# Kernel optimization log

Measured on AMD Instinct MI355X. Metric: run time of the kernel, lower is better.

Reference implementation:

```python
import jax, jax.numpy as jnp
import numpy as np

N_EMBD = 384
BLOCK_SIZE = 256

def setup_inputs() -> dict:
    key = jax.random.key(0)
    k1, k2 = jax.random.split(key)
    B, T = 512, 256
    x = jax.random.normal(k1, (B, T, N_EMBD), dtype=jnp.float32)
    # nn.Linear(384, 192, bias=False): store as [in, out] so projection is x @ w
    w_qkv = jax.random.normal(k2, (N_EMBD, 3 * 64), dtype=jnp.float32) * (1.0 / np.sqrt(N_EMBD))
    return {"x": x, "w_qkv": w_qkv}

def reference(x, w_qkv):
    B, T, C = x.shape  # C == n_embd == 384
    qkv = jnp.einsum('btc,cd->btd', x, w_qkv)       # [B,T,3*hs]
    q, k, v = jnp.split(qkv, 3, axis=-1)            # each [B,T,hs]
    scale = 1.0 / jnp.sqrt(jnp.float32(C))          # NOTE: scales by full embed dim C, per source
    wei = jnp.einsum('btd,bsd->bts', q, k) * scale  # [B,T,T]
    causal = jnp.tril(jnp.ones((T, T), dtype=bool))
    wei = jnp.where(causal, wei, -jnp.inf)
    wei = jax.nn.softmax(wei, axis=-1)
    # dropout is identity in eval mode
    return jnp.einsum('bts,bsd->btd', wei, v)       # [B,T,hs]
```

## Files before the change

### kernel.cpp

```cpp
#include <hip/hip_runtime.h>


constexpr int B  = 512;
constexpr int T  = 256;
constexpr int C  = 384;
constexpr int HS = 64;
constexpr int NT = 192;
constexpr int VP = 264;
constexpr float SCALE = 0.05103103630798288f;
constexpr float QSC   = SCALE * 1.4426950408889634f;

typedef _Float16 f16x8 __attribute__((ext_vector_type(8)));
typedef _Float16 f16x4 __attribute__((ext_vector_type(4)));
typedef __fp16   fp16x2_raw __attribute__((ext_vector_type(2)));
typedef float    f32x4 __attribute__((ext_vector_type(4)));

#if defined(__has_builtin)
#if __has_builtin(__builtin_amdgcn_exp2f)
#define EXP2F(v) __builtin_amdgcn_exp2f(v)
#endif
#endif
#ifndef EXP2F
#define EXP2F(v) exp2f(v)
#endif

__global__ __launch_bounds__(256)
void wt_kernel(const float* __restrict__ w, _Float16* __restrict__ wt) {
    const int idx = blockIdx.x * 256 + threadIdx.x;
    if (idx < NT * C) {
        const int n = idx / C, k = idx % C;
        wt[idx] = (_Float16)w[k * NT + n];
    }
}

__global__ __launch_bounds__(512)
void fused_kernel(const float* __restrict__ x, const _Float16* __restrict__ wt,
                  float* __restrict__ out) {
    __shared__ __align__(16) char arena[NT * C * 2];
    _Float16* const QL  = (_Float16*)arena;
    _Float16* const KL  = (_Float16*)(arena + 32768);
    _Float16* const VTL = (_Float16*)(arena + 65536);

    const int tid  = threadIdx.x;
    const int lane = tid & 63, wv = tid >> 6;
    const int l15  = lane & 15, quad = lane >> 4;
    const int swz  = (l15 & 7) << 4;
    const int q16  = quad << 4;
    const float* xb = x + (long)blockIdx.x * T * C;

#pragma unroll
    for (int i = 0; i < 18; ++i) {
        const int u = tid + 512 * i;
        const int n = u / 48, sl = u - n * 48;
        const uint4 wv4 = *(const uint4*)((const char*)wt + (long)u * 16);
        *(uint4*)(arena + n * 768 + ((sl * 16) ^ ((n & 7) << 4))) = wv4;
    }

    const float* pA0 = xb + (wv * 32 + l15) * C + quad * 8;
    const float* pA1 = xb + (wv * 32 + 16 + l15) * C + quad * 8;

    f32x4 ax[2][2][2];
    ax[0][0][0] = *(const f32x4*)(pA0 + 0);
    ax[0][0][1] = *(const f32x4*)(pA0 + 4);
    ax[0][1][0] = *(const f32x4*)(pA1 + 0);
    ax[0][1][1] = *(const f32x4*)(pA1 + 4);

    f32x4 acc[2][12];
#pragma unroll
    for (int mi = 0; mi < 2; ++mi)
#pragma unroll
        for (int ni = 0; ni < 12; ++ni) acc[mi][ni] = (f32x4)0.f;

    int rowb[12];
#pragma unroll
    for (int ni = 0; ni < 12; ++ni) rowb[ni] = (ni * 16 + l15) * 768;

    __syncthreads();

#pragma unroll
    for (int t = 0; t < 12; ++t) {
        const int cur = t & 1, nxt = cur ^ 1;
        if (t < 11) {
            ax[nxt][0][0] = *(const f32x4*)(pA0 + (t + 1) * 32);
            ax[nxt][0][1] = *(const f32x4*)(pA0 + (t + 1) * 32 + 4);
            ax[nxt][1][0] = *(const f32x4*)(pA1 + (t + 1) * 32);
            ax[nxt][1][1] = *(const f32x4*)(pA1 + (t + 1) * 32 + 4);
        }
        f16x8 af[2];
#pragma unroll
        for (int mi = 0; mi < 2; ++mi) {
            union { fp16x2_raw h[4]; f16x8 v; } cu;
            cu.h[0] = __builtin_amdgcn_cvt_pkrtz(ax[cur][mi][0][0], ax[cur][mi][0][1]);
            cu.h[1] = __builtin_amdgcn_cvt_pkrtz(ax[cur][mi][0][2], ax[cur][mi][0][3]);
            cu.h[2] = __builtin_amdgcn_cvt_pkrtz(ax[cur][mi][1][0], ax[cur][mi][1][1]);
            cu.h[3] = __builtin_amdgcn_cvt_pkrtz(ax[cur][mi][1][2], ax[cur][mi][1][3]);
            af[mi] = cu.v;
        }
        const int col = ((t * 64) + q16) ^ swz;
#pragma unroll
        for (int ni = 0; ni < 12; ++ni) {
            const f16x8 bf = *(const f16x8*)(arena + rowb[ni] + col);
            acc[0][ni] = __builtin_amdgcn_mfma_f32_16x16x32_f16(af[0], bf, acc[0][ni], 0, 0, 0);
            acc[1][ni] = __builtin_amdgcn_mfma_f32_16x16x32_f16(af[1], bf, acc[1][ni], 0, 0, 0);
        }
    }

    __syncthreads();

#pragma unroll
    for (int mi = 0; mi < 2; ++mi) {
        const int t0 = wv * 32 + mi * 16 + quad * 4;
#pragma unroll
        for (int ni = 0; ni < 12; ++ni) {
            const int colbase = ni * 16;
            const int col = colbase + l15;
            if (colbase < 64) {
#pragma unroll
                for (int r = 0; r < 4; ++r) {
                    const int tq = t0 + r;
                    QL[(tq * HS + col) ^ ((tq & 7) << 3)] =
                        (_Float16)(acc[mi][ni][r] * QSC);
                }
            } else if (colbase < 128) {
#pragma unroll
                for (int r = 0; r < 4; ++r) {
                    const int tq = t0 + r;
                    KL[(tq * HS + (col - 64)) ^ ((tq & 7) << 3)] =
                        (_Float16)acc[mi][ni][r];
                }
            } else {
                f16x4 pv;
#pragma unroll
                for (int r = 0; r < 4; ++r) pv[r] = (_Float16)acc[mi][ni][r];
                *(f16x4*)&VTL[(col - 128) * VP + t0] = pv;
            }
        }
    }
    __syncthreads();

    float* ob = out + (long)blockIdx.x * T * HS;
#pragma unroll
    for (int pass = 0; pass < 2; ++pass) {
        const int ch = pass ? (15 - wv) : wv;
        const int q0 = ch * 16;
        const int qrow = q0 + l15;
        const f16x8 qf0 = *(const f16x8*)&QL[(qrow * HS + quad * 8) ^ ((qrow & 7) << 3)];
        const f16x8 qf1 = *(const f16x8*)&QL[(qrow * HS + 32 + quad * 8) ^ ((qrow & 7) << 3)];
        f32x4 o[4];
#pragma unroll
        for (int di = 0; di < 4; ++di) o[di] = (f32x4)0.f;
        float lp = 0.f;

        for (int kt = 0; kt <= ch; ++kt) {
            const int k0 = kt * 16;
            const int krow = k0 + l15;
            const f16x8 ka0 = *(const f16x8*)&KL[(krow * HS + quad * 8) ^ ((krow & 7) << 3)];
            const f16x8 ka1 = *(const f16x8*)&KL[(krow * HS + 32 + quad * 8) ^ ((krow & 7) << 3)];
            f16x4 va[4];
#pragma unroll
            for (int di = 0; di < 4; ++di)
                va[di] = *(const f16x4*)&VTL[(di * 16 + l15) * VP + k0 + quad * 4];

            f32x4 s = {0.f, 0.f, 0.f, 0.f};
            s = __builtin_amdgcn_mfma_f32_16x16x32_f16(ka0, qf0, s, 0, 0, 0);
            s = __builtin_amdgcn_mfma_f32_16x16x32_f16(ka1, qf1, s, 0, 0, 0);

            const bool dmask = (kt == ch);
            f16x4 pb; float psum = 0.f;
#pragma unroll
            for (int r = 0; r < 4; ++r) {
                float pr = EXP2F(s[r]);
                pr = (dmask && (quad * 4 + r > l15)) ? 0.f : pr;
                psum += pr;
                pb[r] = (_Float16)pr;
            }
            lp += psum;
#pragma unroll
            for (int di = 0; di < 4; ++di)
                o[di] = __builtin_amdgcn_mfma_f32_16x16x16f16(va[di], pb, o[di], 0, 0, 0);
        }

        float v = lp;
        v += __shfl_xor(v, 16, 64);
        v += __shfl_xor(v, 32, 64);
        const float inv = 1.0f / v;
#pragma unroll
        for (int di = 0; di < 4; ++di) {
            float4 val;
            val.x = o[di][0] * inv; val.y = o[di][1] * inv;
            val.z = o[di][2] * inv; val.w = o[di][3] * inv;
            *(float4*)&ob[qrow * HS + di * 16 + quad * 4] = val;
        }
    }
}

extern "C" void kernel_launch(void* const* d_in, const int* in_sizes, int n_in,
                              void* d_out, int out_size, void* d_ws, size_t ws_size,
                              hipStream_t stream) {
    const float* x = (const float*)d_in[0];
    const float* w = (const float*)d_in[1];
    float* out = (float*)d_out;

    _Float16* wt = (_Float16*)d_ws;

    wt_kernel<<<dim3((NT * C + 255) / 256), dim3(256), 0, stream>>>(w, wt);
    fused_kernel<<<dim3(B), dim3(512), 0, stream>>>(x, wt, out);
}
```

Before: 299.6 us.

## Process two batches per block and prefetch next batch during attention

```diff
diff --git a/kernel.cpp b/kernel.cpp
--- a/kernel.cpp
+++ b/kernel.cpp
@@ -46,102 +46,106 @@
     const int l15  = lane & 15, quad = lane >> 4;
     const int swz  = (l15 & 7) << 4;
     const int q16  = quad << 4;
-    const float* xb = x + (long)blockIdx.x * T * C;
-
-#pragma unroll
-    for (int i = 0; i < 18; ++i) {
-        const int u = tid + 512 * i;
-        const int n = u / 48, sl = u - n * 48;
-        const uint4 wv4 = *(const uint4*)((const char*)wt + (long)u * 16);
-        *(uint4*)(arena + n * 768 + ((sl * 16) ^ ((n & 7) << 4))) = wv4;
-    }
-
-    const float* pA0 = xb + (wv * 32 + l15) * C + quad * 8;
-    const float* pA1 = xb + (wv * 32 + 16 + l15) * C + quad * 8;
-
-    f32x4 ax[2][2][2];
-    ax[0][0][0] = *(const f32x4*)(pA0 + 0);
-    ax[0][0][1] = *(const f32x4*)(pA0 + 4);
-    ax[0][1][0] = *(const f32x4*)(pA1 + 0);
-    ax[0][1][1] = *(const f32x4*)(pA1 + 4);
-
+    const long b0  = (long)blockIdx.x * 2;
+    const float* xb0 = x + b0 * T * C;
+    const float* xb1 = xb0 + (long)T * C;
+
+    int rowb[12];
+#pragma unroll
+    for (int ni = 0; ni < 12; ++ni) rowb[ni] = (ni * 16 + l15) * 768;
+
+    uint4 wreg[18];
+    f32x4 ax[3][4];
     f32x4 acc[2][12];
-#pragma unroll
-    for (int mi = 0; mi < 2; ++mi)
-#pragma unroll
-        for (int ni = 0; ni < 12; ++ni) acc[mi][ni] = (f32x4)0.f;
-
-    int rowb[12];
-#pragma unroll
-    for (int ni = 0; ni < 12; ++ni) rowb[ni] = (ni * 16 + l15) * 768;
-
-    __syncthreads();
-
-#pragma unroll
-    for (int t = 0; t < 12; ++t) {
-        const int cur = t & 1, nxt = cur ^ 1;
-        if (t < 11) {
-            ax[nxt][0][0] = *(const f32x4*)(pA0 + (t + 1) * 32);
-            ax[nxt][0][1] = *(const f32x4*)(pA0 + (t + 1) * 32 + 4);
-            ax[nxt][1][0] = *(const f32x4*)(pA1 + (t + 1) * 32);
-            ax[nxt][1][1] = *(const f32x4*)(pA1 + (t + 1) * 32 + 4);
-        }
-        f16x8 af[2];
+
+    auto wload = [&]() {
+#pragma unroll
+        for (int i = 0; i < 18; ++i)
+            wreg[i] = *(const uint4*)((const char*)wt + (long)(tid + 512 * i) * 16);
+    };
+    auto wstore = [&]() {
+#pragma unroll
+        for (int i = 0; i < 18; ++i) {
+            const int u = tid + 512 * i;
+            const int n = u / 48, sl = u - n * 48;
+            *(uint4*)(arena + n * 768 + ((sl * 16) ^ ((n & 7) << 4))) = wreg[i];
+        }
+    };
+    auto prime = [&](const float* xbb) {
+        const float* p0 = xbb + (wv * 32 + l15) * C + quad * 8;
+        const float* p1 = p0 + 16 * C;
+        ax[0][0] = *(const f32x4*)(p0);      ax[0][1] = *(const f32x4*)(p0 + 4);
+        ax[0][2] = *(const f32x4*)(p1);      ax[0][3] = *(const f32x4*)(p1 + 4);
+        ax[1][0] = *(const f32x4*)(p0 + 32); ax[1][1] = *(const f32x4*)(p0 + 36);
+        ax[1][2] = *(const f32x4*)(p1 + 32); ax[1][3] = *(const f32x4*)(p1 + 36);
+    };
+    auto kloop = [&](const float* xbb) {
+        const float* p0 = xbb + (wv * 32 + l15) * C + quad * 8;
+        const float* p1 = p0 + 16 * C;
+#pragma unroll
+        for (int mi = 0; mi < 2; ++mi)
+#pragma unroll
+            for (int ni = 0; ni < 12; ++ni) acc[mi][ni] = (f32x4)0.f;
+#pragma unroll
+        for (int t = 0; t < 12; ++t) {
+            const int cur = t % 3, pre = (t + 2) % 3;
+            if (t < 10) {
+                ax[pre][0] = *(const f32x4*)(p0 + (t + 2) * 32);
+                ax[pre][1] = *(const f32x4*)(p0 + (t + 2) * 32 + 4);
+                ax[pre][2] = *(const f32x4*)(p1 + (t + 2) * 32);
+                ax[pre][3] = *(const f32x4*)(p1 + (t + 2) * 32 + 4);
+            }
+            f16x8 af[2];
+#pragma unroll
+            for (int mi = 0; mi < 2; ++mi) {
+                union { fp16x2_raw h[4]; f16x8 v; } cu;
+                cu.h[0] = __builtin_amdgcn_cvt_pkrtz(ax[cur][2*mi][0], ax[cur][2*mi][1]);
+                cu.h[1] = __builtin_amdgcn_cvt_pkrtz(ax[cur][2*mi][2], ax[cur][2*mi][3]);
+                cu.h[2] = __builtin_amdgcn_cvt_pkrtz(ax[cur][2*mi+1][0], ax[cur][2*mi+1][1]);
+                cu.h[3] = __builtin_amdgcn_cvt_pkrtz(ax[cur][2*mi+1][2], ax[cur][2*mi+1][3]);
+                af[mi] = cu.v;
+            }
+            const int col = (t * 64 + q16) ^ swz;
+#pragma unroll
+            for (int ni = 0; ni < 12; ++ni) {
+                const f16x8 bf = *(const f16x8*)(arena + rowb[ni] + col);
+                acc[0][ni] = __builtin_amdgcn_mfma_f32_16x16x32_f16(af[0], bf, acc[0][ni], 0, 0, 0);
+                acc[1][ni] = __builtin_amdgcn_mfma_f32_16x16x32_f16(af[1], bf, acc[1][ni], 0, 0, 0);
+            }
+        }
+    };
+    auto epi = [&]() {
 #pragma unroll
         for (int mi = 0; mi < 2; ++mi) {
-            union { fp16x2_raw h[4]; f16x8 v; } cu;
-            cu.h[0] = __builtin_amdgcn_cvt_pkrtz(ax[cur][mi][0][0], ax[cur][mi][0][1]);
-            cu.h[1] = __builtin_amdgcn_cvt_pkrtz(ax[cur][mi][0][2], ax[cur][mi][0][3]);
-            cu.h[2] = __builtin_amdgcn_cvt_pkrtz(ax[cur][mi][1][0], ax[cur][mi][1][1]);
-            cu.h[3] = __builtin_amdgcn_cvt_pkrtz(ax[cur][mi][1][2], ax[cur][mi][1][3]);
-            af[mi] = cu.v;
-        }
-        const int col = ((t * 64) + q16) ^ swz;
-#pragma unroll
-        for (int ni = 0; ni < 12; ++ni) {
-            const f16x8 bf = *(const f16x8*)(arena + rowb[ni] + col);
-            acc[0][ni] = __builtin_amdgcn_mfma_f32_16x16x32_f16(af[0], bf, acc[0][ni], 0, 0, 0);
-            acc[1][ni] = __builtin_amdgcn_mfma_f32_16x16x32_f16(af[1], bf, acc[1][ni], 0, 0, 0);
-        }
-    }
-
-    __syncthreads();
-
-#pragma unroll
-    for (int mi = 0; mi < 2; ++mi) {
-        const int t0 = wv * 32 + mi * 16 + quad * 4;
-#pragma unroll
-        for (int ni = 0; ni < 12; ++ni) {
-            const int colbase = ni * 16;
-            const int col = colbase + l15;
-            if (colbase < 64) {
-#pragma unroll
-                for (int r = 0; r < 4; ++r) {
-                    const int tq = t0 + r;
-                    QL[(tq * HS + col) ^ ((tq & 7) << 3)] =
-                        (_Float16)(acc[mi][ni][r] * QSC);
+            const int t0 = wv * 32 + mi * 16 + quad * 4;
+#pragma unroll
+            for (int ni = 0; ni < 12; ++ni) {
+                const int colbase = ni * 16;
+                const int col = colbase + l15;
+                if (colbase < 64) {
+#pragma unroll
+                    for (int r = 0; r < 4; ++r) {
+                        const int tq = t0 + r;
+                        QL[(tq * HS + col) ^ ((tq & 7) << 3)] =
+                            (_Float16)(acc[mi][ni][r] * QSC);
+                    }
+                } else if (colbase < 128) {
+#pragma unroll
+                    for (int r = 0; r < 4; ++r) {
+                        const int tq = t0 + r;
+                        KL[(tq * HS + (col - 64)) ^ ((tq & 7) << 3)] =
+                            (_Float16)acc[mi][ni][r];
+                    }
+                } else {
+                    f16x4 pv;
+#pragma unroll
+                    for (int r = 0; r < 4; ++r) pv[r] = (_Float16)acc[mi][ni][r];
+                    *(f16x4*)&VTL[(col - 128) * VP + t0] = pv;
                 }
-            } else if (colbase < 128) {
-#pragma unroll
-                for (int r = 0; r < 4; ++r) {
-                    const int tq = t0 + r;
-                    KL[(tq * HS + (col - 64)) ^ ((tq & 7) << 3)] =
-                        (_Float16)acc[mi][ni][r];
-                }
-            } else {
-                f16x4 pv;
-#pragma unroll
-                for (int r = 0; r < 4; ++r) pv[r] = (_Float16)acc[mi][ni][r];
-                *(f16x4*)&VTL[(col - 128) * VP + t0] = pv;
-            }
-        }
-    }
-    __syncthreads();
-
-    float* ob = out + (long)blockIdx.x * T * HS;
-#pragma unroll
-    for (int pass = 0; pass < 2; ++pass) {
-        const int ch = pass ? (15 - wv) : wv;
+            }
+        }
+    };
+    auto p2pass = [&](int ch, float* ob) {
         const int q0 = ch * 16;
         const int qrow = q0 + l15;
         const f16x8 qf0 = *(const f16x8*)&QL[(qrow * HS + quad * 8) ^ ((qrow & 7) << 3)];
@@ -191,7 +195,31 @@
             val.z = o[di][2] * inv; val.w = o[di][3] * inv;
             *(float4*)&ob[qrow * HS + di * 16 + quad * 4] = val;
         }
-    }
+    };
+
+    float* ob0 = out + b0 * T * HS;
+    float* ob1 = ob0 + (long)T * HS;
+
+    wload(); prime(xb0);
+    wstore();
+    __syncthreads();
+    kloop(xb0);
+    __syncthreads();
+    epi();
+    __syncthreads();
+    p2pass(wv, ob0);
+    wload(); prime(xb1);
+    p2pass(15 - wv, ob0);
+    __syncthreads();
+
+    wstore();
+    __syncthreads();
+    kloop(xb1);
+    __syncthreads();
+    epi();
+    __syncthreads();
+    p2pass(wv, ob1);
+    p2pass(15 - wv, ob1);
 }
 
 extern "C" void kernel_launch(void* const* d_in, const int* in_sizes, int n_in,
@@ -204,5 +232,5 @@
     _Float16* wt = (_Float16*)d_ws;
 
     wt_kernel<<<dim3((NT * C + 255) / 256), dim3(256), 0, stream>>>(w, wt);
-    fused_kernel<<<dim3(B), dim3(512), 0, stream>>>(x, wt, out);
+    fused_kernel<<<dim3(B / 2), dim3(512), 0, stream>>>(x, wt, out);
 }
```

After: 327.5 us. 9.3% more time.
